# Optimization experiments

Measured on AMD Instinct MI355X. Metric: run time of the kernel, lower is better.

The kernel has to match this reference:

```python
import jax, jax.numpy as jnp
import numpy as np

N_NODES = 50000
N_EDGES = 600000
IN_CH, HID1, HID2, OUT_CH = 128, 256, 128, 2


def setup_inputs() -> dict:
    key = jax.random.key(0)
    ks = jax.random.split(key, 8)
    x = jax.random.normal(ks[0], (N_NODES, IN_CH), dtype=jnp.float32)
    edge_index = jax.random.randint(ks[1], (2, N_EDGES), 0, N_NODES, dtype=jnp.int64)
    # Glorot-style init for GCN linear weights
    def glorot(k, fan_in, fan_out):
        s = jnp.sqrt(6.0 / (fan_in + fan_out)).astype(jnp.float32)
        return jax.random.uniform(k, (fan_in, fan_out), jnp.float32, -s, s)
    return {
        "x": x,
        "W1": glorot(ks[2], IN_CH, HID1), "b1": jnp.zeros((HID1,), jnp.float32),
        "W2": glorot(ks[3], HID1, HID2), "b2": jnp.zeros((HID2,), jnp.float32),
        "W3": glorot(ks[4], HID2, OUT_CH), "b3": jnp.zeros((OUT_CH,), jnp.float32),
        "edge_index": edge_index,
    }


def _gcn_graph(edge_index, n_nodes):
    # Add self-loops (GCNConv default) and compute symmetric normalization
    loop = jnp.arange(n_nodes, dtype=edge_index.dtype)
    src = jnp.concatenate([edge_index[0], loop])
    dst = jnp.concatenate([edge_index[1], loop])
    ones = jnp.ones(src.shape[0], dtype=jnp.float32)
    deg = jax.ops.segment_sum(ones, dst, num_segments=n_nodes)
    dinv = jnp.where(deg > 0, jax.lax.rsqrt(deg), 0.0)
    norm = dinv[src] * dinv[dst]  # [E + N]
    return src, dst, norm


def _gcn_layer(h, W, b, src, dst, norm, n_nodes):
    h = h @ W                                   # [N, d_out]
    msg = h[src] * norm[:, None]                # gather + scale  [E+N, d_out]
    agg = jax.ops.segment_sum(msg, dst, num_segments=n_nodes)
    return agg + b


def reference(x, W1, b1, W2, b2, W3, b3, edge_index):
    n = x.shape[0]
    src, dst, norm = _gcn_graph(edge_index, n)
    h = jax.nn.relu(_gcn_layer(x, W1, b1, src, dst, norm, n))
    # dropout p=0.5 is identity in eval mode (training=False)
    h = jax.nn.relu(_gcn_layer(h, W2, b2, src, dst, norm, n))
    h = _gcn_layer(h, W3, b3, src, dst, norm, n)
    return jax.nn.log_softmax(h, axis=1)
```

## Files before the change

### kernel.cpp

```cpp
#include <hip/hip_runtime.h>
#include <hip/hip_bf16.h>
#include <math.h>

#define N_NODES 50000
#define N_EDGES 600000
#define E_TOT   (N_EDGES + N_NODES)
#define M_PAD   50048
#define CSR_CAP 1400192

typedef __attribute__((ext_vector_type(8))) short bf16x8;
typedef __attribute__((ext_vector_type(4))) float f32x4;
typedef __attribute__((ext_vector_type(8))) unsigned short u16x8;


__device__ __forceinline__ unsigned short f2bf(float f) {
    unsigned int u = __float_as_uint(f);
    unsigned int r = (u + 0x7fffu + ((u >> 16) & 1u)) >> 16;
    return (unsigned short)r;
}

__device__ __forceinline__ void acc_row(float* acc, uint4 v) {
    acc[0] += __uint_as_float(v.x << 16);
    acc[1] += __uint_as_float(v.x & 0xffff0000u);
    acc[2] += __uint_as_float(v.y << 16);
    acc[3] += __uint_as_float(v.y & 0xffff0000u);
    acc[4] += __uint_as_float(v.z << 16);
    acc[5] += __uint_as_float(v.z & 0xffff0000u);
    acc[6] += __uint_as_float(v.w << 16);
    acc[7] += __uint_as_float(v.w & 0xffff0000u);
}

#define GLD_LDS16(g, l) __builtin_amdgcn_global_load_lds( \
    (__attribute__((address_space(1))) void*)(void*)(g), \
    (__attribute__((address_space(3))) void*)(l), 16, 0, 0)


__global__ void prep_kernel(const int* __restrict__ ei, int* __restrict__ cnt,
                            const float* __restrict__ W1, const float* __restrict__ W2,
                            unsigned short* __restrict__ W1t, unsigned short* __restrict__ W2t) {
    const int NB_E = (N_EDGES + 255) / 256;
    int b = blockIdx.x;
    if (b < NB_E) {
        int e = b * 256 + threadIdx.x;
        if (e < N_EDGES) atomicAdd(&cnt[ei[N_EDGES + e]], 1);
    } else if (b < NB_E + 128) {
        int i = (b - NB_E) * 256 + threadIdx.x;
        int k = i >> 8, n = i & 255;
        W1t[(size_t)n * 128 + k] = f2bf(W1[i]);
    } else {
        int i = (b - NB_E - 128) * 256 + threadIdx.x;
        int k = i >> 7, n = i & 127;
        W2t[(size_t)n * 256 + k] = f2bf(W2[i]);
    }
}


__global__ __launch_bounds__(256) void scan_kernel(
    const int* __restrict__ cnt, float* __restrict__ dinv,
    int* __restrict__ row_ptr, int* __restrict__ blockSum,
    const float* __restrict__ x, unsigned short* __restrict__ xs) {
    const int NB_S = (N_NODES + 255) / 256;
    const int NB_C = (N_NODES * 32 + 255) / 256;
    int b = blockIdx.x;
    int tid = threadIdx.x;
    if (b < NB_S) {
        __shared__ int sdata[256];
        __shared__ int s_prefix;
        int i = b * 256 + tid;
        int deg = (i < N_NODES) ? (cnt[i] + 1) : 0;
        if (i < N_NODES) dinv[i] = rsqrtf((float)deg);
        int v = (i < N_NODES) ? ((deg + 15) & ~15) : 0;
        sdata[tid] = v;
        __syncthreads();
        #pragma unroll
        for (int off = 1; off < 256; off <<= 1) {
            int t = (tid >= off) ? sdata[tid - off] : 0;
            __syncthreads();
            sdata[tid] += t;
            __syncthreads();
        }
        if (tid == 0) atomicExch(&blockSum[b], sdata[255]);
        if (tid < 64) {
            int sum = 0;
            for (int j = tid; j < b; j += 64) {
                int vj;
                do { vj = atomicAdd(&blockSum[j], 0); } while (vj == 0);
                sum += vj;
            }
            #pragma unroll
            for (int off = 1; off < 64; off <<= 1) sum += __shfl_xor(sum, off);
            if (tid == 0) s_prefix = sum;
        }
        __syncthreads();
        int prefix = s_prefix;
        if (i < N_NODES) row_ptr[i] = prefix + sdata[tid] - v;
        if (i == N_NODES - 1) row_ptr[N_NODES] = prefix + sdata[tid];
    } else if (b < NB_S + NB_C) {
        int i = (b - NB_S) * 256 + tid;
        if (i >= N_NODES * 32) return;
        float d = rsqrtf((float)(cnt[i >> 5] + 1));
        float4 v = *(const float4*)(x + (size_t)i * 4);
        ushort4 o;
        o.x = f2bf(v.x * d); o.y = f2bf(v.y * d); o.z = f2bf(v.z * d); o.w = f2bf(v.w * d);
        *(ushort4*)(xs + (size_t)i * 4) = o;
    } else {
        if (tid < 16)
            *(uint4*)(xs + (size_t)N_NODES * 128 + tid * 8) = make_uint4(0, 0, 0, 0);
    }
}


__global__ void fill_kernel(const int* __restrict__ ei, const int* __restrict__ cnt,
                            const int* __restrict__ row_ptr, int* __restrict__ fill,
                            unsigned short* __restrict__ csr) {
    const int NB_A = (E_TOT + 255) / 256;
    const int NB_B = (N_NODES + 255) / 256;
    int b = blockIdx.x;
    if (b < NB_A) {
        int e = b * 256 + threadIdx.x;
        if (e >= E_TOT) return;
        int s, d;
        if (e < N_EDGES) { s = ei[e]; d = ei[N_EDGES + e]; }
        else             { s = d = e - N_EDGES; }
        int pos = row_ptr[d] + atomicAdd(&fill[d], 1);
        csr[pos] = (unsigned short)s;
    } else if (b < NB_A + NB_B) {
        int i = (b - NB_A) * 256 + threadIdx.x;
        if (i >= N_NODES) return;
        int start = row_ptr[i] + cnt[i] + 1;
        int end = row_ptr[i + 1];
        for (int j = start; j < end; ++j) csr[j] = (unsigned short)N_NODES;
    } else {
        int t = threadIdx.x;
        if (t < 128) csr[row_ptr[N_NODES] + t] = (unsigned short)N_NODES;
    }
}


template<bool LAYER2>
__global__ __launch_bounds__(256) void agg_kernel(
    const unsigned short* __restrict__ Hs, const float* __restrict__ dinv,
    const int* __restrict__ row_ptr, const unsigned short* __restrict__ csr,
    const float* __restrict__ bias, const float* __restrict__ W3,
    unsigned short* __restrict__ outb, float2* __restrict__ Ts) {
    int wave = threadIdx.x >> 6;
    int lane = threadIdx.x & 63;
    int n = blockIdx.x * 4 + wave;
    if (LAYER2 && blockIdx.x == 0 && threadIdx.x == 0) Ts[N_NODES] = make_float2(0.f, 0.f);
    if (n >= N_NODES) return;
    int quarter = lane >> 4;
    int q = lane & 15;
    float acc[8] = {};
    int p0 = row_ptr[n], p1 = row_ptr[n + 1];
    int p = p0 + quarter * 4;
    ushort4 s4 = *(const ushort4*)(csr + p);
    while (p < p1) {
        int pn = p + 16;
        ushort4 n4 = *(const ushort4*)(csr + pn);
        uint4 v0 = *(const uint4*)(Hs + (size_t)s4.x * 128 + q * 8);
        uint4 v1 = *(const uint4*)(Hs + (size_t)s4.y * 128 + q * 8);
        uint4 v2 = *(const uint4*)(Hs + (size_t)s4.z * 128 + q * 8);
        uint4 v3 = *(const uint4*)(Hs + (size_t)s4.w * 128 + q * 8);
        acc_row(acc, v0);
        acc_row(acc, v1);
        acc_row(acc, v2);
        acc_row(acc, v3);
        p = pn; s4 = n4;
    }
    #pragma unroll
    for (int i = 0; i < 8; ++i) {
        acc[i] += __shfl_xor(acc[i], 16);
        acc[i] += __shfl_xor(acc[i], 32);
    }
    float dn = dinv[n];
    if (!LAYER2) {
        if (quarter == 0) {
            u16x8 ov;
            #pragma unroll
            for (int i = 0; i < 8; ++i) ov[i] = f2bf(acc[i] * dn);
            *(u16x8*)(outb + (size_t)n * 128 + q * 8) = ov;
        }
    } else {
        float t0 = 0.f, t1 = 0.f;
        #pragma unroll
        for (int i = 0; i < 8; ++i) {
            int c = q * 8 + i;
            float h = fmaxf(acc[i] * dn + bias[c], 0.f);
            float2 w = ((const float2*)W3)[c];
            t0 += h * w.x; t1 += h * w.y;
        }
        #pragma unroll
        for (int off = 1; off < 16; off <<= 1) {
            t0 += __shfl_xor(t0, off);
            t1 += __shfl_xor(t1, off);
        }
        if (lane == 0) Ts[n] = make_float2(t0 * dn, t1 * dn);
    }
}


__global__ __launch_bounds__(256) void gemm12_kernel(
    const unsigned short* __restrict__ A,
    const unsigned short* __restrict__ W1t,
    const unsigned short* __restrict__ W2t,
    const float* __restrict__ b1,
    const float* __restrict__ rowscale,
    unsigned short* __restrict__ C,
    int M) {
    __shared__ __align__(16) unsigned short h1buf[128 * 256];
    __shared__ __align__(16) unsigned short As[128 * 32];
    __shared__ __align__(16) unsigned short Bs[64 * 32];
    int tid = threadIdx.x;
    int wave = tid >> 6, lane = tid & 63;
    int m0 = blockIdx.x * 128;
    int mm = lane & 15, kg = lane >> 4;
    int row0 = kg * 4;

    int am[2];
    #pragma unroll
    for (int i = 0; i < 2; ++i) {
        int m = wave * 32 + i * 16 + mm;
        am[i] = (m * 4 + (kg ^ ((m >> 1) & 3))) * 8;
    }
    int bn[4];
    #pragma unroll
    for (int j = 0; j < 4; ++j) {
        int n = j * 16 + mm;
        bn[j] = (n * 4 + (kg ^ ((n >> 1) & 3))) * 8;
    }
    int h1rd[2];
    #pragma unroll
    for (int i = 0; i < 2; ++i) {
        int m = wave * 32 + i * 16 + mm;
        h1rd[i] = m * 32 * 8;
    }

    #pragma unroll 1
    for (int nt = 0; nt < 4; ++nt) {
        int n0 = nt * 64;
        f32x4 acc[2][4];
        #pragma unroll
        for (int i = 0; i < 2; ++i)
            #pragma unroll
            for (int j = 0; j < 4; ++j)
                acc[i][j] = (f32x4){0.f, 0.f, 0.f, 0.f};
        #pragma unroll 1
        for (int k0 = 0; k0 < 128; k0 += 32) {
            #pragma unroll
            for (int iss = 0; iss < 2; ++iss) {
                int ci = iss * 256 + tid;
                int r = ci >> 2, c8s = ci & 3;
                int c8 = c8s ^ ((r >> 1) & 3);
                const unsigned short* g = A + (size_t)(m0 + r) * 128 + k0 + c8 * 8;
                unsigned short* l = As + (size_t)(iss * 256 + (tid & 192)) * 8;
                GLD_LDS16(g, l);
            }
            {
                int r = tid >> 2, c8s = tid & 3;
                int c8 = c8s ^ ((r >> 1) & 3);
                const unsigned short* g = W1t + (size_t)(n0 + r) * 128 + k0 + c8 * 8;
                unsigned short* l = Bs + (size_t)(tid & 192) * 8;
                GLD_LDS16(g, l);
            }
            __syncthreads();
            bf16x8 af[2], bfr[4];
            #pragma unroll
            for (int i = 0; i < 2; ++i) af[i] = *(const bf16x8*)(As + am[i]);
            #pragma unroll
            for (int j = 0; j < 4; ++j) bfr[j] = *(const bf16x8*)(Bs + bn[j]);
            #pragma unroll
            for (int i = 0; i < 2; ++i)
                #pragma unroll
                for (int j = 0; j < 4; ++j)
                    acc[i][j] = __builtin_amdgcn_mfma_f32_16x16x32_bf16(af[i], bfr[j], acc[i][j], 0, 0, 0);
            __syncthreads();
        }
        float bj[4];
        #pragma unroll
        for (int j = 0; j < 4; ++j) bj[j] = b1[n0 + j * 16 + mm];
        #pragma unroll
        for (int i = 0; i < 2; ++i) {
            #pragma unroll
            for (int r = 0; r < 4; ++r) {
                int ml = wave * 32 + i * 16 + row0 + r;
                int rb = ml * 32 * 8, rx = ml & 15;
                #pragma unroll
                for (int j = 0; j < 4; ++j) {
                    int c = n0 + j * 16 + mm;
                    int c8 = c >> 3;
                    float v = fmaxf(acc[i][j][r] + bj[j], 0.f);
                    h1buf[rb + ((c8 ^ rx) * 8) + (c & 7)] = f2bf(v);
                }
            }
        }
    }
    __syncthreads();

    #pragma unroll 1
    for (int nh = 0; nh < 2; ++nh) {
        int n0 = nh * 64;
        f32x4 acc[2][4];
        #pragma unroll
        for (int i = 0; i < 2; ++i)
            #pragma unroll
            for (int j = 0; j < 4; ++j)
                acc[i][j] = (f32x4){0.f, 0.f, 0.f, 0.f};
        #pragma unroll 1
        for (int k0 = 0; k0 < 256; k0 += 32) {
            {
                int r = tid >> 2, c8s = tid & 3;
                int c8 = c8s ^ ((r >> 1) & 3);
                const unsigned short* g = W2t + (size_t)(n0 + r) * 256 + k0 + c8 * 8;
                unsigned short* l = Bs + (size_t)(tid & 192) * 8;
                GLD_LDS16(g, l);
            }
            __syncthreads();
            bf16x8 af[2], bfr[4];
            #pragma unroll
            for (int i = 0; i < 2; ++i) {
                int m = wave * 32 + i * 16 + mm;
                int c8 = (k0 >> 3) + kg;
                af[i] = *(const bf16x8*)(h1buf + h1rd[i] + ((c8 ^ (m & 15)) * 8));
            }
            #pragma unroll
            for (int j = 0; j < 4; ++j) bfr[j] = *(const bf16x8*)(Bs + bn[j]);
            #pragma unroll
            for (int i = 0; i < 2; ++i)
                #pragma unroll
                for (int j = 0; j < 4; ++j)
                    acc[i][j] = __builtin_amdgcn_mfma_f32_16x16x32_bf16(af[i], bfr[j], acc[i][j], 0, 0, 0);
            __syncthreads();
        }
        #pragma unroll
        for (int i = 0; i < 2; ++i) {
            #pragma unroll
            for (int r = 0; r < 4; ++r) {
                int gm = m0 + wave * 32 + i * 16 + row0 + r;
                float sc = (gm < M) ? rowscale[gm] : 0.f;
                #pragma unroll
                for (int j = 0; j < 4; ++j) {
                    int gn = n0 + j * 16 + mm;
                    C[(size_t)gm * 128 + gn] = f2bf(acc[i][j][r] * sc);
                }
            }
        }
    }
}


__global__ void lsm_kernel(const float2* __restrict__ Ts, const float* __restrict__ dinv,
                           const int* __restrict__ row_ptr, const unsigned short* __restrict__ csr,
                           const float* __restrict__ b3, float* __restrict__ out) {
    int n = blockIdx.x * 256 + threadIdx.x;
    if (n >= N_NODES) return;
    float a0 = 0.f, a1 = 0.f;
    int p0 = row_ptr[n], p1 = row_ptr[n + 1];
    ushort4 s4 = *(const ushort4*)(csr + p0);
    for (int p = p0; p < p1; p += 4) {
        ushort4 n4 = *(const ushort4*)(csr + p + 4);
        float2 u0 = Ts[s4.x], u1 = Ts[s4.y], u2 = Ts[s4.z], u3 = Ts[s4.w];
        a0 += (u0.x + u1.x) + (u2.x + u3.x);
        a1 += (u0.y + u1.y) + (u2.y + u3.y);
        s4 = n4;
    }
    float dn = dinv[n];
    float v0 = a0 * dn + b3[0];
    float v1 = a1 * dn + b3[1];
    float m = fmaxf(v0, v1);
    float lse = m + logf(expf(v0 - m) + expf(v1 - m));
    out[n * 2 + 0] = v0 - lse;
    out[n * 2 + 1] = v1 - lse;
}


extern "C" void kernel_launch(void* const* d_in, const int* in_sizes, int n_in,
                              void* d_out, int out_size, void* d_ws, size_t ws_size,
                              hipStream_t stream) {
    const float* x  = (const float*)d_in[0];
    const float* W1 = (const float*)d_in[1];
    const float* b1 = (const float*)d_in[2];
    const float* W2 = (const float*)d_in[3];
    const float* b2 = (const float*)d_in[4];
    const float* W3 = (const float*)d_in[5];
    const float* b3 = (const float*)d_in[6];
    const int*   ei = (const int*)d_in[7];
    float* out = (float*)d_out;

    char* ws = (char*)d_ws;
    size_t off = 0;
    auto alloc = [&](size_t bytes) -> char* {
        char* p = ws + off;
        off = (off + bytes + 255) & ~(size_t)255;
        return p;
    };
    int*   cnt      = (int*)alloc(N_NODES * 4);
    int*   fill     = (int*)alloc(N_NODES * 4);
    int*   blockSum = (int*)alloc(256 * 4);
    char*  zero_end = ws + off;
    float* dinv    = (float*)alloc(N_NODES * 4);
    int*   row_ptr = (int*)alloc((N_NODES + 1) * 4);
    unsigned short* csr = (unsigned short*)alloc(CSR_CAP * 2);
    unsigned short* xs     = (unsigned short*)alloc((size_t)(N_NODES + 1) * 128 * 2);
    unsigned short* W1t    = (unsigned short*)alloc((size_t)256 * 128 * 2);
    unsigned short* W2t    = (unsigned short*)alloc((size_t)128 * 256 * 2);
    unsigned short* aggx_b = (unsigned short*)alloc((size_t)M_PAD * 128 * 2);
    unsigned short* t2b    = (unsigned short*)alloc((size_t)M_PAD * 128 * 2);
    float2* Ts = (float2*)alloc((size_t)(N_NODES + 1) * 8);

    hipMemsetAsync(cnt, 0, (size_t)(zero_end - (char*)cnt), stream);

    int nb = (N_NODES + 255) / 256;
    const int NB_E = (N_EDGES + 255) / 256;
    prep_kernel<<<NB_E + 256, 256, 0, stream>>>(ei, cnt, W1, W2, W1t, W2t);
    const int NB_C = (N_NODES * 32 + 255) / 256;
    scan_kernel<<<nb + NB_C + 1, 256, 0, stream>>>(cnt, dinv, row_ptr, blockSum, x, xs);
    const int NB_A = (E_TOT + 255) / 256;
    fill_kernel<<<NB_A + nb + 1, 256, 0, stream>>>(ei, cnt, row_ptr, fill, csr);

    agg_kernel<false><<<(N_NODES + 3) / 4, 256, 0, stream>>>(
        xs, dinv, row_ptr, csr, nullptr, nullptr, aggx_b, nullptr);
    gemm12_kernel<<<M_PAD / 128, 256, 0, stream>>>(
        aggx_b, W1t, W2t, b1, dinv, t2b, N_NODES);
    agg_kernel<true><<<(N_NODES + 3) / 4, 256, 0, stream>>>(
        t2b, dinv, row_ptr, csr, b2, W3, nullptr, Ts);

    lsm_kernel<<<(N_NODES + 255) / 256, 256, 0, stream>>>(Ts, dinv, row_ptr, csr, b3, out);
}
```

Before: 234.3 us.

## Merge graph-build kernels and memset into one cooperative kernel with grid syncs

Replaces the memset plus the prep, scan and fill kernels with a single cooperative kernel of 1024 blocks that uses grid-stride loops and grid.sync between phases. The aim is to remove three kernel launches and a memset, along with their launch gaps. In exchange, occupancy is limited to a fixed grid, and grid-wide barriers plus a cooperative launch add their own cost. The scan phase still relies on the first 196 blocks spinning on blockSum, which requires all of them to be co-resident.

```diff
diff --git a/kernel.cpp b/kernel.cpp
--- a/kernel.cpp
+++ b/kernel.cpp
@@ -1,6 +1,9 @@
 #include <hip/hip_runtime.h>
 #include <hip/hip_bf16.h>
+#include <hip/hip_cooperative_groups.h>
 #include <math.h>
+
+namespace cg = cooperative_groups;
 
 #define N_NODES 50000
 #define N_EDGES 600000
@@ -35,37 +38,38 @@
     (__attribute__((address_space(3))) void*)(l), 16, 0, 0)
 
 
-__global__ void prep_kernel(const int* __restrict__ ei, int* __restrict__ cnt,
-                            const float* __restrict__ W1, const float* __restrict__ W2,
-                            unsigned short* __restrict__ W1t, unsigned short* __restrict__ W2t) {
-    const int NB_E = (N_EDGES + 255) / 256;
-    int b = blockIdx.x;
-    if (b < NB_E) {
-        int e = b * 256 + threadIdx.x;
-        if (e < N_EDGES) atomicAdd(&cnt[ei[N_EDGES + e]], 1);
-    } else if (b < NB_E + 128) {
-        int i = (b - NB_E) * 256 + threadIdx.x;
+__global__ __launch_bounds__(256, 4) void build_kernel(
+    const int* __restrict__ ei, int* __restrict__ cnt, int* __restrict__ fillc,
+    int* __restrict__ blockSum,
+    const float* __restrict__ W1, const float* __restrict__ W2,
+    unsigned short* __restrict__ W1t, unsigned short* __restrict__ W2t,
+    float* __restrict__ dinv, int* __restrict__ row_ptr,
+    unsigned short* __restrict__ csr,
+    const float* __restrict__ x, unsigned short* __restrict__ xs) {
+    cg::grid_group grid = cg::this_grid();
+    __shared__ int sdata[256];
+    __shared__ int s_prefix;
+    int b = blockIdx.x, tid = threadIdx.x;
+    int g = b * 256 + tid;
+    int GSZ = gridDim.x << 8;
+
+    for (int i = g; i < N_NODES; i += GSZ) { cnt[i] = 0; fillc[i] = 0; }
+    if (g < 256) blockSum[g] = 0;
+    grid.sync();
+
+    for (int i = g; i < N_EDGES; i += GSZ) atomicAdd(&cnt[ei[N_EDGES + i]], 1);
+    for (int i = g; i < 128 * 256; i += GSZ) {
         int k = i >> 8, n = i & 255;
         W1t[(size_t)n * 128 + k] = f2bf(W1[i]);
-    } else {
-        int i = (b - NB_E - 128) * 256 + threadIdx.x;
+    }
+    for (int i = g; i < 256 * 128; i += GSZ) {
         int k = i >> 7, n = i & 127;
         W2t[(size_t)n * 256 + k] = f2bf(W2[i]);
     }
-}
-
-
-__global__ __launch_bounds__(256) void scan_kernel(
-    const int* __restrict__ cnt, float* __restrict__ dinv,
-    int* __restrict__ row_ptr, int* __restrict__ blockSum,
-    const float* __restrict__ x, unsigned short* __restrict__ xs) {
-    const int NB_S = (N_NODES + 255) / 256;
-    const int NB_C = (N_NODES * 32 + 255) / 256;
-    int b = blockIdx.x;
-    int tid = threadIdx.x;
-    if (b < NB_S) {
-        __shared__ int sdata[256];
-        __shared__ int s_prefix;
+    if (g < 16) *(uint4*)(xs + (size_t)N_NODES * 128 + g * 8) = make_uint4(0, 0, 0, 0);
+    grid.sync();
+
+    if (b < 196) {
         int i = b * 256 + tid;
         int deg = (i < N_NODES) ? (cnt[i] + 1) : 0;
         if (i < N_NODES) dinv[i] = rsqrtf((float)deg);
@@ -95,45 +99,29 @@
         int prefix = s_prefix;
         if (i < N_NODES) row_ptr[i] = prefix + sdata[tid] - v;
         if (i == N_NODES - 1) row_ptr[N_NODES] = prefix + sdata[tid];
-    } else if (b < NB_S + NB_C) {
-        int i = (b - NB_S) * 256 + tid;
-        if (i >= N_NODES * 32) return;
+    }
+    for (int i = g; i < N_NODES * 32; i += GSZ) {
         float d = rsqrtf((float)(cnt[i >> 5] + 1));
         float4 v = *(const float4*)(x + (size_t)i * 4);
         ushort4 o;
         o.x = f2bf(v.x * d); o.y = f2bf(v.y * d); o.z = f2bf(v.z * d); o.w = f2bf(v.w * d);
         *(ushort4*)(xs + (size_t)i * 4) = o;
-    } else {
-        if (tid < 16)
-            *(uint4*)(xs + (size_t)N_NODES * 128 + tid * 8) = make_uint4(0, 0, 0, 0);
-    }
-}
-
-
-__global__ void fill_kernel(const int* __restrict__ ei, const int* __restrict__ cnt,
-                            const int* __restrict__ row_ptr, int* __restrict__ fill,
-                            unsigned short* __restrict__ csr) {
-    const int NB_A = (E_TOT + 255) / 256;
-    const int NB_B = (N_NODES + 255) / 256;
-    int b = blockIdx.x;
-    if (b < NB_A) {
-        int e = b * 256 + threadIdx.x;
-        if (e >= E_TOT) return;
+    }
+    grid.sync();
+
+    for (int e = g; e < E_TOT; e += GSZ) {
         int s, d;
         if (e < N_EDGES) { s = ei[e]; d = ei[N_EDGES + e]; }
         else             { s = d = e - N_EDGES; }
-        int pos = row_ptr[d] + atomicAdd(&fill[d], 1);
+        int pos = row_ptr[d] + atomicAdd(&fillc[d], 1);
         csr[pos] = (unsigned short)s;
-    } else if (b < NB_A + NB_B) {
-        int i = (b - NB_A) * 256 + threadIdx.x;
-        if (i >= N_NODES) return;
+    }
+    for (int i = g; i < N_NODES; i += GSZ) {
         int start = row_ptr[i] + cnt[i] + 1;
         int end = row_ptr[i + 1];
         for (int j = start; j < end; ++j) csr[j] = (unsigned short)N_NODES;
-    } else {
-        int t = threadIdx.x;
-        if (t < 128) csr[row_ptr[N_NODES] + t] = (unsigned short)N_NODES;
-    }
+    }
+    if (g < 128) csr[row_ptr[N_NODES] + g] = (unsigned short)N_NODES;
 }
 
 
@@ -394,9 +382,8 @@
         return p;
     };
     int*   cnt      = (int*)alloc(N_NODES * 4);
-    int*   fill     = (int*)alloc(N_NODES * 4);
+    int*   fillc    = (int*)alloc(N_NODES * 4);
     int*   blockSum = (int*)alloc(256 * 4);
-    char*  zero_end = ws + off;
     float* dinv    = (float*)alloc(N_NODES * 4);
     int*   row_ptr = (int*)alloc((N_NODES + 1) * 4);
     unsigned short* csr = (unsigned short*)alloc(CSR_CAP * 2);
@@ -407,15 +394,13 @@
     unsigned short* t2b    = (unsigned short*)alloc((size_t)M_PAD * 128 * 2);
     float2* Ts = (float2*)alloc((size_t)(N_NODES + 1) * 8);
 
-    hipMemsetAsync(cnt, 0, (size_t)(zero_end - (char*)cnt), stream);
-
-    int nb = (N_NODES + 255) / 256;
-    const int NB_E = (N_EDGES + 255) / 256;
-    prep_kernel<<<NB_E + 256, 256, 0, stream>>>(ei, cnt, W1, W2, W1t, W2t);
-    const int NB_C = (N_NODES * 32 + 255) / 256;
-    scan_kernel<<<nb + NB_C + 1, 256, 0, stream>>>(cnt, dinv, row_ptr, blockSum, x, xs);
-    const int NB_A = (E_TOT + 255) / 256;
-    fill_kernel<<<NB_A + nb + 1, 256, 0, stream>>>(ei, cnt, row_ptr, fill, csr);
+    void* kargs[] = {
+        (void*)&ei, (void*)&cnt, (void*)&fillc, (void*)&blockSum,
+        (void*)&W1, (void*)&W2, (void*)&W1t, (void*)&W2t,
+        (void*)&dinv, (void*)&row_ptr, (void*)&csr, (void*)&x, (void*)&xs
+    };
+    hipLaunchCooperativeKernel((const void*)build_kernel, dim3(1024), dim3(256),
+                               kargs, 0, stream);
 
     agg_kernel<false><<<(N_NODES + 3) / 4, 256, 0, stream>>>(
         xs, dinv, row_ptr, csr, nullptr, nullptr, aggx_b, nullptr);
```

Measured after the change: 528.2 us. 125% more time.
